# Kernel optimization log

Hardware: AMD Instinct MI355X
Metric: run time of the kernel (lower is better)

Reference implementation:

```python
import jax, jax.numpy as jnp
import numpy as np

B, T = 64, 512          # batch, seq_len
D = 512                 # model_size / LSTM hidden
V = 256                 # vocab_size
R, W, M = 4, 16, 5      # read_heads, cell_size, nr_cells
RW = R * W
IFC = R * W + 3 * W + 5 * R + 3   # DNC interface vector size = 135
EPS = 1e-6
CLIP = 20.0


def setup_inputs():
    ks = jax.random.split(jax.random.key(0), 12)
    s = 0.05
    f32 = jnp.float32
    return {
        'tokens':   jax.random.randint(ks[0], (B, T), 0, V, dtype=jnp.int32),
        'emb':      jax.random.normal(ks[1], (V, D), f32),
        'lstm_Wi0': jax.random.normal(ks[2], (4 * D, D + RW), f32) * s,
        'lstm_Wh0': jax.random.normal(ks[3], (4 * D, D), f32) * s,
        'lstm_b0':  jnp.zeros((4 * D,), f32),
        'lstm_Wi1': jax.random.normal(ks[4], (4 * D, D), f32) * s,
        'lstm_Wh1': jax.random.normal(ks[5], (4 * D, D), f32) * s,
        'lstm_b1':  jnp.zeros((4 * D,), f32),
        'W_if':     jax.random.normal(ks[6], (IFC, D), f32) * s,
        'b_if':     jnp.zeros((IFC,), f32),
        'W_out':    jax.random.normal(ks[7], (D, D + RW), f32) * s,
        'b_out':    jnp.zeros((D,), f32),
        'W_fc':     jax.random.normal(ks[8], (V, D), f32) * s,
        'b_fc':     jnp.zeros((V,), f32),
    }


def _cosine(mem, keys):
    # mem (B,M,W), keys (B,K,W) -> (B,K,M) batchwise cosine similarity
    mn = mem / (jnp.linalg.norm(mem, axis=2, keepdims=True) + EPS)
    kn = keys / (jnp.linalg.norm(keys, axis=2, keepdims=True) + EPS)
    return jnp.einsum('bkw,bmw->bkm', kn, mn)


def _allocate(usage):
    # DNC allocation weighting via sort + exclusive cumprod, then unsort
    u = EPS + (1.0 - EPS) * usage                           # (B,M)
    idx = jnp.argsort(u, axis=1)                            # ascending usage
    sorted_u = jnp.take_along_axis(u, idx, axis=1)
    prod_excl = jnp.cumprod(
        jnp.concatenate([jnp.ones_like(u[:, :1]), sorted_u], axis=1), axis=1)[:, :-1]
    alloc_sorted = (1.0 - sorted_u) * prod_excl
    inv = jnp.argsort(idx, axis=1)                          # reverse permutation
    return jnp.take_along_axis(alloc_sorted, inv, axis=1)


def _dnc_forward(tokens, emb, lstm_Wi0, lstm_Wh0, lstm_b0,
                 lstm_Wi1, lstm_Wh1, lstm_b1, W_if, b_if,
                 W_out, b_out, W_fc, b_fc):
    x = emb[tokens]                                         # (B,T,D)
    eye_mask = 1.0 - jnp.eye(M, dtype=x.dtype)

    def lstm_cell(xin, h, c, Wi, Wh, b):
        g = xin @ Wi.T + h @ Wh.T + b
        i, f, gg, o = jnp.split(g, 4, axis=1)               # torch gate order i,f,g,o
        c2 = jax.nn.sigmoid(f) * c + jax.nn.sigmoid(i) * jnp.tanh(gg)
        h2 = jax.nn.sigmoid(o) * jnp.tanh(c2)
        return h2, c2

    def step(carry, x_t):
        h0, c0, h1, c1, mem, link, prec, rw_p, ww_p, usage, last_read = carry
        xin = jnp.concatenate([x_t, last_read], axis=1)     # (B, D+RW)
        nh0, nc0 = lstm_cell(xin, h0, c0, lstm_Wi0, lstm_Wh0, lstm_b0)
        nh1, nc1 = lstm_cell(nh0, h1, c1, lstm_Wi1, lstm_Wh1, lstm_b1)
        out = jnp.clip(nh1, -CLIP, CLIP)
        xi = out @ W_if.T + b_if                            # (B, IFC)

        o = 0
        read_keys = jnp.tanh(xi[:, :RW]).reshape(-1, R, W); o = RW
        read_str  = jax.nn.softplus(xi[:, o:o + R]); o += R
        write_key = jnp.tanh(xi[:, o:o + W]); o += W
        write_str = jax.nn.softplus(xi[:, o]); o += 1
        erase     = jax.nn.sigmoid(xi[:, o:o + W]); o += W
        write_vec = jnp.tanh(xi[:, o:o + W]); o += W
        free_g    = jax.nn.sigmoid(xi[:, o:o + R]); o += R
        alloc_g   = jax.nn.sigmoid(xi[:, o]); o += 1
        write_g   = jax.nn.sigmoid(xi[:, o]); o += 1
        read_modes = jax.nn.softmax(xi[:, o:o + 3 * R].reshape(-1, R, 3), axis=-1)

        # ---- write head ----
        usage2 = usage + (1.0 - usage) * ww_p               # single write head
        psi = jnp.prod(1.0 - free_g[:, :, None] * rw_p, axis=1)   # (B,M)
        usage2 = usage2 * psi
        wcw = jax.nn.softmax(
            _cosine(mem, write_key[:, None, :])[:, 0, :] * write_str[:, None], axis=1)
        alloc = _allocate(usage2)
        ww = write_g[:, None] * (alloc_g[:, None] * alloc
                                 + (1.0 - alloc_g[:, None]) * wcw)  # (B,M)
        mem2 = mem * (1.0 - ww[:, :, None] * erase[:, None, :]) \
               + ww[:, :, None] * write_vec[:, None, :]
        link2 = (1.0 - ww[:, :, None] - ww[:, None, :]) * link \
                + ww[:, :, None] * prec[:, None, :]
        link2 = link2 * eye_mask
        prec2 = (1.0 - jnp.sum(ww, axis=1, keepdims=True)) * prec + ww

        # ---- read heads ----
        rcw = jax.nn.softmax(_cosine(mem2, read_keys) * read_str[:, :, None], axis=2)
        fwd = jnp.einsum('bij,brj->bri', link2, rw_p)       # L @ w_prev
        bwd = jnp.einsum('bij,bri->brj', link2, rw_p)       # L^T @ w_prev
        rw = (read_modes[..., 0:1] * bwd + read_modes[..., 1:2] * fwd
              + read_modes[..., 2:3] * rcw)                 # (B,R,M)
        read_vecs = jnp.einsum('brm,bmw->brw', rw, mem2).reshape(-1, RW)

        y = jnp.concatenate([out, read_vecs], axis=1) @ W_out.T + b_out  # (B,D)
        carry = (nh0, nc0, nh1, nc1, mem2, link2, prec2, rw, ww, usage2, read_vecs)
        return carry, y

    b = tokens.shape[0]
    z = lambda *shape: jnp.zeros(shape, x.dtype)
    carry0 = (z(b, D), z(b, D), z(b, D), z(b, D),
              z(b, M, W), z(b, M, M), z(b, M),
              z(b, R, M), z(b, M), z(b, M), z(b, RW))
    _, ys = jax.lax.scan(step, carry0, jnp.swapaxes(x, 0, 1))
    y = jnp.swapaxes(ys, 0, 1)                              # (B,T,D)
    logits = y @ W_fc.T + b_fc                              # (B,T,V)
    return jnp.transpose(logits, (0, 2, 1))                 # (B,V,T)


def reference(tokens, emb, lstm_Wi0, lstm_Wh0, lstm_b0,
              lstm_Wi1, lstm_Wh1, lstm_b1, W_if, b_if,
              W_out, b_out, W_fc, b_fc):
    return _dnc_forward(tokens, emb, lstm_Wi0, lstm_Wh0, lstm_b0,
                        lstm_Wi1, lstm_Wh1, lstm_b1, W_if, b_if,
                        W_out, b_out, W_fc, b_fc)
```

## Files before the change

### kernel.cpp

```cpp
#include <hip/hip_runtime.h>
#include <hip/hip_bf16.h>

typedef __hip_bfloat16 bf16;
typedef _Float16 f16;
typedef _Float16 f16x8 __attribute__((ext_vector_type(8)));
typedef float f32x4 __attribute__((ext_vector_type(4)));
typedef unsigned long long u64;
typedef unsigned short ushort_t;

__device__ __forceinline__ float b2f(bf16 x){ return __bfloat162float(x); }
__device__ __forceinline__ float sigf(float x){ return 1.f/(1.f+expf(-x)); }
__device__ __forceinline__ float splus(float x){ return fmaxf(x,0.f)+log1pf(expf(-fabsf(x))); }
__device__ __forceinline__ float ldf(const void* p, int i, int isf32){
  return isf32 ? ((const float*)p)[i] : __bfloat162float(((const bf16*)p)[i]);
}
__device__ __forceinline__ void ast64(u64* p, u64 v){ __hip_atomic_store(p, v, __ATOMIC_RELAXED, __HIP_MEMORY_SCOPE_AGENT); }
__device__ __forceinline__ u64 ald64(u64* p){ return __hip_atomic_load(p, __ATOMIC_RELAXED, __HIP_MEMORY_SCOPE_AGENT); }
__device__ __forceinline__ void ast32(unsigned* p, unsigned v){ __hip_atomic_store(p, v, __ATOMIC_RELAXED, __HIP_MEMORY_SCOPE_AGENT); }
__device__ __forceinline__ unsigned ald32(unsigned* p){ return __hip_atomic_load(p, __ATOMIC_RELAXED, __HIP_MEMORY_SCOPE_AGENT); }

union U4H8 { uint4 u; f16x8 h; };
union U64H4 { u64 u; f16 h[4]; };
union H16 { f16 h; ushort_t s; };

__global__ void k_detect(const void* __restrict__ emb, int* __restrict__ flag){
  __shared__ float mx[256];
  int tid=threadIdx.x;
  float v = fabsf(__bfloat162float(((const bf16*)emb)[tid]));
  mx[tid]=v; __syncthreads();
  for(int s=128;s>0;s>>=1){ if(tid<s) mx[tid]=fmaxf(mx[tid],mx[tid+s]); __syncthreads(); }
  if(tid==0){ flag[0] = (mx[0]>1000.f) ? 1 : 0; flag[1] = 0; }
}

__global__ void k_embW(const void* __restrict__ emb, const void* __restrict__ Wi0,
                       const void* __restrict__ b0,
                       const int* __restrict__ flags, float* __restrict__ embW){
  int f=flags[0];
  int row = blockIdx.x;
  __shared__ float w[512];
  for(int k=threadIdx.x;k<512;k+=256) w[k]=ldf(Wi0,row*576+k,f);
  __syncthreads();
  int v = threadIdx.x;
  float acc=ldf(b0,row,f);
  #pragma unroll 4
  for(int k=0;k<512;k++) acc += ldf(emb,v*512+k,f)*w[k];
  embW[row*256+v]=acc;
}

__global__ void k_wpkA(const void* __restrict__ Wh0, const void* __restrict__ Wi0,
                       const int* __restrict__ flags, ushort_t* __restrict__ PA){
  int f=flags[0];
  int idx=blockIdx.x*256+threadIdx.x;
  if(idx>=1179648) return;
  int j=idx&7, l=(idx>>3)&63, rest=idx>>9;
  int c=rest%18, t2=rest/18, w=t2&7, r=t2>>3;
  int G=w>>1, hh=w&1, m=l&15, q4=l>>4;
  int row=G*512 + r*32 + hh*16 + m;
  int k=c*32 + q4*8 + j;
  float val = (k<512)? ldf(Wh0,row*512+k,f) : ldf(Wi0,row*576+k,f);
  H16 hx; hx.h=(f16)val; PA[idx]=hx.s;
}
__global__ void k_wpkB(const void* __restrict__ Wi1, const void* __restrict__ Wh1,
                       const int* __restrict__ flags, ushort_t* __restrict__ PB){
  int f=flags[0];
  int idx=blockIdx.x*256+threadIdx.x;
  if(idx>=2097152) return;
  int j=idx&7, l=(idx>>3)&63, rest=idx>>9;
  int c=rest&31, t2=rest>>5, w=t2&7, r=t2>>3;
  int G=w>>1, hh=w&1, m=l&15, q4=l>>4;
  int row=G*512 + r*32 + hh*16 + m;
  int k=c*32 + q4*8 + j;
  float val = (k<512)? ldf(Wi1,row*512+k,f) : ldf(Wh1,row*512+k-512,f);
  H16 hx; hx.h=(f16)val; PB[idx]=hx.s;
}

__global__ void k_wifP(const void* __restrict__ W_if, const void* __restrict__ b_if,
                       const int* __restrict__ flags,
                       ushort_t* __restrict__ PW, float* __restrict__ b_ifF,
                       unsigned* __restrict__ FLz){
  int f=flags[0];
  int idx=blockIdx.x*256+threadIdx.x;
  if(idx<73728){
    int j=idx&7, l=(idx>>3)&63, c=(idx>>9)&15, tile=idx>>13;
    int row=tile*16+(l&15);
    int k=c*32+(l>>4)*8+j;
    float val=(row<135)? ldf(W_if,row*512+k,f) : 0.f;
    H16 hx; hx.h=(f16)val; PW[idx]=hx.s;
  }
  if(idx<64) FLz[idx]=0u;
  if(idx<135) b_ifF[idx]=ldf(b_if,idx,f);
}

__global__ void k_wc(const void* __restrict__ W_fc, const void* __restrict__ W_out,
                     const void* __restrict__ b_out, const void* __restrict__ b_fc,
                     const int* __restrict__ flags,
                     float* __restrict__ Wc, float* __restrict__ bc){
  int f=flags[0];
  int idx=blockIdx.x*256+threadIdx.x;
  int v=idx/576, j=idx-v*576;
  float acc=0.f;
  #pragma unroll 4
  for(int d=0;d<512;d++) acc += ldf(W_fc,v*512+d,f)*ldf(W_out,d*576+j,f);
  Wc[idx]=acc;
  if(j==0){
    float a=ldf(b_fc,v,f);
    for(int d=0;d<512;d++) a += ldf(W_fc,v*512+d,f)*ldf(b_out,d,f);
    bc[v]=a;
  }
}

__attribute__((amdgpu_waves_per_eu(2,2)))
__global__ void __launch_bounds__(512) k_dnc3(
    const int* __restrict__ tokens, const void* __restrict__ b1, const int* __restrict__ flags,
    const float* __restrict__ embW, const ushort_t* __restrict__ PA, const ushort_t* __restrict__ PB,
    const ushort_t* __restrict__ PW, const float* __restrict__ b_ifF,
    u64* GX0, u64* GX1, unsigned* FL,
    bf16* __restrict__ cat)
{
  const int bid = blockIdx.x;
  const int g   = bid>>4, r = bid&15;
  const int tid = threadIdx.x;
  const int wv  = tid>>6, l = tid&63;
  const int lm  = l&15,  q4 = l>>4;
  const int d   = tid>>4, bb = tid&15;
  const int mb  = tid>>5, mu = tid&31;
  const int f32i = flags[0];

  __shared__ __align__(16) u64 HB[4352];
  __shared__ float PR[128*17];
  __shared__ f16  sh_pub[512];
  __shared__ float sh_b1[128];
  __shared__ float b_ifL[144];
  __shared__ float xis2[16*149];
  __shared__ float s_mem[1280], s_mem2[1280], s_link[400], s_link2[400];
  __shared__ float s_prec[80], s_prec2[80], s_rwp[320], s_rw[320];
  __shared__ float s_wwp[80], s_ww[80], s_usage[80], s_wl[80];
  __shared__ float s_rl[320], s_fwd[320], s_bwd[320], s_wsum[16];
  __shared__ float rvbuf[1024];

#define WAITG(TGT) do{ if(tid<16){ unsigned _tg=(unsigned)(TGT); int _wd=0; \
    while(ald32(&FL[g*16+tid]) < _tg && _wd<50000000){ __builtin_amdgcn_s_sleep(1); _wd++; } } \
  __syncthreads(); }while(0)
#define PUBF(VAL) do{ __syncthreads(); \
  if(tid==0) ast32(&FL[g*16+r],(unsigned)(VAL)); }while(0)
#define XI(i) xis2[mb*149+(i)]

  f16x8 fa[18], fb[32];
  {
    const uint4* PAv=(const uint4*)PA;
    const uint4* PBv=(const uint4*)PB;
    #pragma unroll
    for(int c=0;c<18;c++){ U4H8 t4; t4.u = PAv[((r*8+wv)*18+c)*64 + l]; fa[c]=t4.h; }
    #pragma unroll
    for(int c=0;c<32;c++){ U4H8 t4; t4.u = PBv[((r*8+wv)*32+c)*64 + l]; fb[c]=t4.h; }
    #pragma unroll
    for(int c=0;c<18;c++) asm volatile("" :: "v"(fa[c]));
    #pragma unroll
    for(int c=0;c<32;c++) asm volatile("" :: "v"(fb[c]));
  }
  if(tid<128) sh_b1[tid]=ldf(b1,(tid>>5)*512 + r*32 + (tid&31), f32i);
  if(tid<144) b_ifL[tid]=(tid<135)? b_ifF[tid] : 0.f;
  for(int i=tid;i<1280;i+=512) s_mem[i]=0.f;
  for(int i=tid;i<400;i+=512) s_link[i]=0.f;
  for(int i=tid;i<320;i+=512) s_rwp[i]=0.f;
  if(tid<80){ s_prec[tid]=0.f; s_wwp[tid]=0.f; s_usage[tid]=0.f; }
  float c0s=0.f, c1s=0.f;

  const f16x8* HBv=(const f16x8*)HB;
  const uint4* PWv=(const uint4*)PW;

  {
    int tok0=tokens[(g*16+bb)*512];
    int base0=(r*32+d)*256+tok0;
    float e0=embW[base0], e2=embW[262144+base0], e3=embW[393216+base0];
    c0s = sigf(e0)*tanhf(e2);
    float h0v = sigf(e3)*tanhf(c0s);
    sh_pub[d*16+bb]=(f16)h0v;
  }
  __syncthreads();
  if(tid<128){
    int ks=tid>>4, b2=tid&15;
    U64H4 pk;
    #pragma unroll
    for(int i=0;i<4;i++) pk.h[i]=sh_pub[(ks*4+i)*16+b2];
    ast64(&GX0[g*4096+((4*r+(ks>>1))*16+b2)*2+(ks&1)], pk.u);
  }
  PUBF(2u);
  WAITG(2u);
  {
    u64 s0=ald64(&GX0[g*4096+tid      ]);
    u64 s1=ald64(&GX0[g*4096+tid+512  ]);
    u64 s2=ald64(&GX0[g*4096+tid+1024 ]);
    u64 s3=ald64(&GX0[g*4096+tid+1536 ]);
    HB[tid]=s0; HB[tid+512]=s1; HB[tid+1024]=s2; HB[tid+1536]=s3;
  }
  __syncthreads();
  {
    f32x4 accB=(f32x4){0.f,0.f,0.f,0.f};
    #pragma unroll
    for(int c=0;c<16;c++){
      f16x8 bfr=HBv[(c*4+q4)*16+lm];
      accB=__builtin_amdgcn_mfma_f32_16x16x32_f16(fb[c],bfr,accB,0,0,0);
    }
    #pragma unroll
    for(int reg=0;reg<4;reg++) PR[(wv*16+q4*4+reg)*17+lm]=accB[reg];
  }
  __syncthreads();
  {
    float gi=PR[(d    )*17+bb]+sh_b1[d];
    float gg=PR[(64+d )*17+bb]+sh_b1[64+d];
    float go=PR[(96+d )*17+bb]+sh_b1[96+d];
    c1s = sigf(gi)*tanhf(gg);
    float h=sigf(go)*tanhf(c1s);
    sh_pub[d*16+bb]=(f16)h;
  }
  __syncthreads();
  if(tid<128){
    int ks=tid>>4, b2=tid&15;
    U64H4 pk;
    #pragma unroll
    for(int i=0;i<4;i++) pk.h[i]=sh_pub[(ks*4+i)*16+b2];
    ast64(&GX1[g*4096+((4*r+(ks>>1))*16+b2)*2+(ks&1)], pk.u);
  }
  PUBF(3u);

  for(int tt=0;tt<512;tt++){
    const int p=tt&1, pn=p^1;

    f32x4 accA=(f32x4){0.f,0.f,0.f,0.f};
    #pragma unroll
    for(int c=0;c<16;c++){
      f16x8 bfr=HBv[(c*4+q4)*16+lm];
      accA=__builtin_amdgcn_mfma_f32_16x16x32_f16(fa[c],bfr,accA,0,0,0);
    }
    float em0,em1,em2,em3;
    {
      int tn=(tt<511)?tt+1:511;
      int tok=tokens[(g*16+bb)*512+tn];
      int base=(r*32+d)*256+tok;
      em0=embW[base]; em1=embW[131072+base]; em2=embW[262144+base]; em3=embW[393216+base];
    }

    WAITG(2*tt+3);

    {
      u64 s0=ald64(&GX1[g*4096+p*2048+tid      ]);
      u64 s1=ald64(&GX1[g*4096+p*2048+tid+512  ]);
      u64 s2=ald64(&GX1[g*4096+p*2048+tid+1024 ]);
      u64 s3=ald64(&GX1[g*4096+p*2048+tid+1536 ]);
      HB[2048+tid]=s0; HB[2048+tid+512]=s1; HB[2048+tid+1024]=s2; HB[2048+tid+1536]=s3;
    }
    __syncthreads();

    {
      f32x4 xa=(f32x4){0.f,0.f,0.f,0.f};
      #pragma unroll
      for(int hh=0;hh<4;hh++){
        uint4 w4[4];
        #pragma unroll
        for(int cc=0;cc<4;cc++) w4[cc]=PWv[(wv*16 + hh*4+cc)*64 + l];
        #pragma unroll
        for(int cc=0;cc<4;cc++){
          U4H8 t4; t4.u=w4[cc];
          f16x8 bfr=HBv[1024+((hh*4+cc)*4+q4)*16+lm];
          xa=__builtin_amdgcn_mfma_f32_16x16x32_f16(t4.h,bfr,xa,0,0,0);
        }
      }
      #pragma unroll
      for(int reg=0;reg<4;reg++){
        int row=wv*16+q4*4+reg;
        xis2[lm*149+row]=xa[reg]+b_ifL[row];
      }
      if(wv==0){
        f32x4 xb=(f32x4){0.f,0.f,0.f,0.f};
        #pragma unroll
        for(int hh=0;hh<4;hh++){
          uint4 w4[4];
          #pragma unroll
          for(int cc=0;cc<4;cc++) w4[cc]=PWv[(128 + hh*4+cc)*64 + l];
          #pragma unroll
          for(int cc=0;cc<4;cc++){
            U4H8 t4; t4.u=w4[cc];
            f16x8 bfr=HBv[1024+((hh*4+cc)*4+q4)*16+lm];
            xb=__builtin_amdgcn_mfma_f32_16x16x32_f16(t4.h,bfr,xb,0,0,0);
          }
        }
        #pragma unroll
        for(int reg=0;reg<4;reg++){
          int row=128+q4*4+reg;
          xis2[lm*149+row]=xb[reg]+b_ifL[row];
        }
      }
    }
    __syncthreads();

    if(mu<5){
      int m=mu;
      float u=s_usage[mb*5+m]+(1.f-s_usage[mb*5+m])*s_wwp[mb*5+m];
      float psi=1.f;
      #pragma unroll
      for(int rr=0;rr<4;rr++) psi *= 1.f - sigf(XI(117+rr))*s_rwp[mb*20+rr*5+m];
      u*=psi; s_usage[mb*5+m]=u;
      float nm=0.f,dt=0.f,nk=0.f;
      #pragma unroll
      for(int w=0;w<16;w++){
        float mv=s_mem[mb*80+m*16+w], kv=tanhf(XI(68+w));
        nm+=mv*mv; dt+=mv*kv; nk+=kv*kv;
      }
      float sim=dt/((sqrtf(nm)+1e-6f)*(sqrtf(nk)+1e-6f));
      s_wl[mb*5+m]=sim*splus(XI(84));
    }
    __syncthreads();
    if(mu==0){
      float mx=-1e30f;
      for(int m=0;m<5;m++) mx=fmaxf(mx,s_wl[mb*5+m]);
      float e[5]; float s=0.f;
      for(int m=0;m<5;m++){ e[m]=expf(s_wl[mb*5+m]-mx); s+=e[m]; }
      float u[5]; int id[5];
      for(int m=0;m<5;m++){ u[m]=1e-6f+(1.f-1e-6f)*s_usage[mb*5+m]; id[m]=m; }
      for(int i=1;i<5;i++){
        float uv=u[i]; int iv=id[i]; int j=i-1;
        while(j>=0&&u[j]>uv){u[j+1]=u[j];id[j+1]=id[j];j--;}
        u[j+1]=uv; id[j+1]=iv;
      }
      float alm[5]; float prod=1.f;
      for(int i=0;i<5;i++){ alm[id[i]]=(1.f-u[i])*prod; prod*=u[i]; }
      float ag=sigf(XI(121)), wgg=sigf(XI(122));
      float wsum=0.f;
      for(int m=0;m<5;m++){
        float wcw=e[m]/s;
        float w_=wgg*(ag*alm[m]+(1.f-ag)*wcw);
        s_ww[mb*5+m]=w_; wsum+=w_;
      }
      s_wsum[mb]=wsum;
    }
    __syncthreads();
    for(int k=mu;k<80;k+=32){
      int m=k>>4,w=k&15;
      float er=sigf(XI(85+w)), wv2=tanhf(XI(101+w));
      float w_=s_ww[mb*5+m];
      s_mem2[mb*80+k]=s_mem[mb*80+k]*(1.f-w_*er)+w_*wv2;
    }
    if(mu<25){
      int i=mu/5, j=mu-5*i;
      s_link2[mb*25+mu]=(i==j)?0.f:((1.f-s_ww[mb*5+i]-s_ww[mb*5+j])*s_link[mb*25+mu]+s_ww[mb*5+i]*s_prec[mb*5+j]);
    } else if(mu<30){
      int j=mu-25;
      s_prec2[mb*5+j]=(1.f-s_wsum[mb])*s_prec[mb*5+j]+s_ww[mb*5+j];
    }
    __syncthreads();
    if(mu<20){
      int rr=mu/5, m=mu-5*rr;
      float nm=0.f,dt=0.f,nk=0.f;
      #pragma unroll
      for(int w=0;w<16;w++){
        float mv=s_mem2[mb*80+m*16+w], kv=tanhf(XI(rr*16+w));
        nm+=mv*mv; dt+=mv*kv; nk+=kv*kv;
      }
      float sim=dt/((sqrtf(nm)+1e-6f)*(sqrtf(nk)+1e-6f));
      s_rl[mb*20+mu]=sim*splus(XI(64+rr));
      float af=0.f, ab=0.f;
      #pragma unroll
      for(int j=0;j<5;j++) af+=s_link2[mb*25+m*5+j]*s_rwp[mb*20+rr*5+j];
      #pragma unroll
      for(int i=0;i<5;i++) ab+=s_link2[mb*25+i*5+m]*s_rwp[mb*20+rr*5+i];
      s_fwd[mb*20+rr*5+m]=af;
      s_bwd[mb*20+rr*5+m]=ab;
    }
    __syncthreads();
    if(mu<20){
      int rr=mu/5;
      float mx=-1e30f;
      for(int m=0;m<5;m++) mx=fmaxf(mx,s_rl[mb*20+rr*5+m]);
      float s=0.f;
      for(int m=0;m<5;m++) s+=expf(s_rl[mb*20+rr*5+m]-mx);
      float rcw=expf(s_rl[mb*20+mu]-mx)/s;
      float q0=XI(123+3*rr),q1=XI(124+3*rr),q2=XI(125+3*rr);
      float m3=fmaxf(q0,fmaxf(q1,q2));
      float e0=expf(q0-m3),e1=expf(q1-m3),e2=expf(q2-m3);
      float inv=1.f/(e0+e1+e2);
      s_rw[mb*20+mu]=(e0*s_bwd[mb*20+mu]+e1*s_fwd[mb*20+mu]+e2*rcw)*inv;
    }
    __syncthreads();
    for(int k=mu;k<64;k+=32){
      int rr=k>>4,w=k&15;
      float a=0.f;
      #pragma unroll
      for(int m=0;m<5;m++) a+=s_rw[mb*20+rr*5+m]*s_mem2[mb*80+m*16+w];
      rvbuf[mb*64+k]=a;
    }
    for(int k=mu;k<80;k+=32) s_mem[mb*80+k]=s_mem2[mb*80+k];
    if(mu<25) s_link[mb*25+mu]=s_link2[mb*25+mu];
    else if(mu<30) s_prec[mb*5+mu-25]=s_prec2[mb*5+mu-25];
    if(mu<20) s_rwp[mb*20+mu]=s_rw[mb*20+mu];
    if(mu>=27&&mu<32){ int m=mu-27; s_wwp[mb*5+m]=s_ww[mb*5+m]; }
    __syncthreads();

    if(tt==511){
      int cb=((g*16+r)*512+tt)*576;
      if(tid<128){
        int kg=tid>>1, e=tid&1;
        U64H4 pv; pv.u=HB[2048+(kg*16+r)*2+e];
        #pragma unroll
        for(int i=0;i<4;i++){
          float x=(float)pv.h[i];
          cat[cb+kg*8+e*4+i]=__float2bfloat16(fminf(fmaxf(x,-20.f),20.f));
        }
      }
      if(tid<64) cat[cb+512+tid]=__float2bfloat16(rvbuf[r*64+tid]);
      break;
    }

    if(tid<256){
      int kg=tid>>5, rem=tid&31, b2=rem>>1, e=rem&1;
      U64H4 pk;
      #pragma unroll
      for(int i=0;i<4;i++) pk.h[i]=(f16)rvbuf[b2*64 + kg*8+e*4+i];
      HB[4096+(kg*16+b2)*2+e]=pk.u;
    }
    __syncthreads();
    #pragma unroll
    for(int c2=0;c2<2;c2++){
      f16x8 bfr=HBv[2048+(c2*4+q4)*16+lm];
      accA=__builtin_amdgcn_mfma_f32_16x16x32_f16(fa[16+c2],bfr,accA,0,0,0);
    }
    #pragma unroll
    for(int reg=0;reg<4;reg++) PR[(wv*16+q4*4+reg)*17+lm]=accA[reg];
    __syncthreads();
    {
      float gi=PR[(d    )*17+bb]+em0;
      float gf=PR[(32+d )*17+bb]+em1;
      float gg=PR[(64+d )*17+bb]+em2;
      float go=PR[(96+d )*17+bb]+em3;
      float c0=sigf(gf)*c0s+sigf(gi)*tanhf(gg);
      c0s=c0;
      float h=sigf(go)*tanhf(c0);
      sh_pub[d*16+bb]=(f16)h;
    }
    __syncthreads();
    if(tid<128){
      int ks=tid>>4, b2=tid&15;
      U64H4 pk;
      #pragma unroll
      for(int i=0;i<4;i++) pk.h[i]=sh_pub[(ks*4+i)*16+b2];
      ast64(&GX0[g*4096+pn*2048+((4*r+(ks>>1))*16+b2)*2+(ks&1)], pk.u);
    }
    PUBF(2*tt+4);

    f32x4 accB=(f32x4){0.f,0.f,0.f,0.f};
    #pragma unroll
    for(int c=16;c<32;c++){
      f16x8 bfr=HBv[1024+((c-16)*4+q4)*16+lm];
      accB=__builtin_amdgcn_mfma_f32_16x16x32_f16(fb[c],bfr,accB,0,0,0);
    }
    {
      int cb=((g*16+r)*512+tt)*576;
      if(tid<128){
        int kg=tid>>1, e=tid&1;
        U64H4 pv; pv.u=HB[2048+(kg*16+r)*2+e];
        #pragma unroll
        for(int i=0;i<4;i++){
          float x=(float)pv.h[i];
          cat[cb+kg*8+e*4+i]=__float2bfloat16(fminf(fmaxf(x,-20.f),20.f));
        }
      }
      if(tid<64) cat[cb+512+tid]=__float2bfloat16(rvbuf[r*64+tid]);
    }

    WAITG(2*tt+4);

    {
      u64 s0=ald64(&GX0[g*4096+pn*2048+tid      ]);
      u64 s1=ald64(&GX0[g*4096+pn*2048+tid+512  ]);
      u64 s2=ald64(&GX0[g*4096+pn*2048+tid+1024 ]);
      u64 s3=ald64(&GX0[g*4096+pn*2048+tid+1536 ]);
      HB[tid]=s0; HB[tid+512]=s1; HB[tid+1024]=s2; HB[tid+1536]=s3;
    }
    __syncthreads();
    #pragma unroll
    for(int c=0;c<16;c++){
      f16x8 bfr=HBv[(c*4+q4)*16+lm];
      accB=__builtin_amdgcn_mfma_f32_16x16x32_f16(fb[c],bfr,accB,0,0,0);
    }
    #pragma unroll
    for(int reg=0;reg<4;reg++) PR[(wv*16+q4*4+reg)*17+lm]=accB[reg];
    __syncthreads();
    {
      float gi=PR[(d    )*17+bb]+sh_b1[d];
      float gf=PR[(32+d )*17+bb]+sh_b1[32+d];
      float gg=PR[(64+d )*17+bb]+sh_b1[64+d];
      float go=PR[(96+d )*17+bb]+sh_b1[96+d];
      float c1=sigf(gf)*c1s+sigf(gi)*tanhf(gg);
      c1s=c1;
      float h=sigf(go)*tanhf(c1);
      sh_pub[d*16+bb]=(f16)h;
    }
    __syncthreads();
    if(tid<128){
      int ks=tid>>4, b2=tid&15;
      U64H4 pk;
      #pragma unroll
      for(int i=0;i<4;i++) pk.h[i]=sh_pub[(ks*4+i)*16+b2];
      ast64(&GX1[g*4096+pn*2048+((4*r+(ks>>1))*16+b2)*2+(ks&1)], pk.u);
    }
    PUBF(2*tt+5);
  }
#undef WAITG
#undef PUBF
#undef XI
}

__global__ void __launch_bounds__(256) k_out(const bf16* __restrict__ cat,
                                             const float* __restrict__ Wc,
                                             const float* __restrict__ bc,
                                             float* __restrict__ outp){
  int t0=blockIdx.x*64, v0=blockIdx.y*64, b=blockIdx.z;
  __shared__ float As[64][33];
  __shared__ float Bs[32][65];
  int tid=threadIdx.x;
  int ti=tid>>4, vi=tid&15;
  float acc[4][4]={};
  for(int k0=0;k0<576;k0+=32){
    for(int i=tid;i<64*32;i+=256){
      int rr=i>>5,k=i&31;
      As[rr][k]=b2f(cat[(b*512+t0+rr)*576+k0+k]);
    }
    for(int i=tid;i<64*32;i+=256){
      int v=i>>5,k=i&31;
      Bs[k][v]=Wc[(v0+v)*576+k0+k];
    }
    __syncthreads();
    #pragma unroll 8
    for(int kk=0;kk<32;kk++){
      float av[4],bv[4];
      #pragma unroll
      for(int x=0;x<4;x++) av[x]=As[ti*4+x][kk];
      #pragma unroll
      for(int y=0;y<4;y++) bv[y]=Bs[kk][vi*4+y];
      #pragma unroll
      for(int x=0;x<4;x++)
        #pragma unroll
        for(int y=0;y<4;y++) acc[x][y]+=av[x]*bv[y];
    }
    __syncthreads();
  }
  #pragma unroll
  for(int y=0;y<4;y++){
    int v=v0+vi*4+y;
    float bcv=bc[v];
    #pragma unroll
    for(int x=0;x<4;x++){
      int tt=t0+ti*4+x;
      outp[(b*256+v)*512+tt]=acc[x][y]+bcv;
    }
  }
}

extern "C" void kernel_launch(void* const* d_in, const int* in_sizes, int n_in,
                              void* d_out, int out_size, void* d_ws, size_t ws_size,
                              hipStream_t stream) {
  const int*  tokens = (const int*) d_in[0];
  const void* emb    = d_in[1];
  const void* Wi0    = d_in[2];
  const void* Wh0    = d_in[3];
  const void* b0     = d_in[4];
  const void* Wi1    = d_in[5];
  const void* Wh1    = d_in[6];
  const void* b1     = d_in[7];
  const void* W_if   = d_in[8];
  const void* b_if   = d_in[9];
  const void* W_out  = d_in[10];
  const void* b_out  = d_in[11];
  const void* W_fc   = d_in[12];
  const void* b_fc   = d_in[13];

  static const int expect[14] = {64*512, 256*512, 2048*576, 2048*512, 2048,
                                 2048*512, 2048*512, 2048, 135*512, 135,
                                 512*576, 512, 256*512, 256};
  bool ok = (n_in == 14);
  if(ok) for(int i=0;i<14;i++) if(in_sizes[i]!=expect[i]) ok=false;

  int*      flags = (int*)d_ws;
  float*    embW  = (float*)d_ws + 64;
  ushort_t* PA    = (ushort_t*)(embW + 524288);
  ushort_t* PB    = PA + 1310720;
  float*    Wreg  = (float*)(PB + 2097152);
  float*    b_ifF = Wreg + 69632;
  float*    Wc    = b_ifF + 160;
  float*    bc    = Wc + 147456;
  u64*      GX0   = (u64*)(bc + 256);
  u64*      GX1   = GX0 + 16384;
  u64*      GXL   = GX1 + 16384;
  bf16*     cat   = (bf16*)(GXL + 2048);
  unsigned* FL    = (unsigned*)(PA + 1179648);
  ushort_t* PW    = (ushort_t*)Wreg;

  size_t need = 9783168ull + 278528ull + 37748736ull;
  if(!ok || ws_size < need){
    hipMemsetAsync(d_out, 0, (size_t)out_size*4, stream);
    return;
  }

  k_detect<<<dim3(1), dim3(256), 0, stream>>>(emb, flags);
  k_embW<<<dim3(2048), dim3(256), 0, stream>>>(emb, Wi0, b0, flags, embW);
  k_wpkA<<<dim3(4608), dim3(256), 0, stream>>>(Wh0, Wi0, flags, PA);
  k_wpkB<<<dim3(8192), dim3(256), 0, stream>>>(Wi1, Wh1, flags, PB);
  k_wifP<<<dim3(288), dim3(256), 0, stream>>>(W_if, b_if, flags, PW, b_ifF, FL);
  k_wc  <<<dim3(576),  dim3(256), 0, stream>>>(W_fc, W_out, b_out, b_fc, flags, Wc, bc);

  void* kargs[] = {
    (void*)&tokens, (void*)&b1, (void*)&flags,
    (void*)&embW, (void*)&PA, (void*)&PB,
    (void*)&PW, (void*)&b_ifF,
    (void*)&GX0, (void*)&GX1, (void*)&FL,
    (void*)&cat
  };
  hipLaunchCooperativeKernel((const void*)k_dnc3, dim3(64), dim3(512), kargs, 0, stream);

  k_out<<<dim3(8,4,64), dim3(256), 0, stream>>>(cat, Wc, bc, (float*)d_out);
}
```

Measured before the change: 13.97 ms.

## Stream LSTM weights from global instead of register-resident, use wave barriers in DNC

Drops the 50 register-resident f16x8 weight fragments (fa/fb) and reloads the LSTM weight tiles from global memory each timestep, with partial prefetch before the waits. This frees a large block of VGPRs. It also parallelises the allocation sort/softmax across lanes using rank-based products, and replaces several block-wide __syncthreads in the per-batch DNC memory section with wave barriers. The cost is repeated weight reads every step through L2/L1, which adds latency on the serial recurrent critical path. The wave-barrier swap assumes each batch's DNC work stays within one wavefront.

```diff
diff --git a/kernel.cpp b/kernel.cpp
--- a/kernel.cpp
+++ b/kernel.cpp
@@ -144,20 +144,13 @@
 #define PUBF(VAL) do{ __syncthreads(); \
   if(tid==0) ast32(&FL[g*16+r],(unsigned)(VAL)); }while(0)
 #define XI(i) xis2[mb*149+(i)]
-
-  f16x8 fa[18], fb[32];
-  {
-    const uint4* PAv=(const uint4*)PA;
-    const uint4* PBv=(const uint4*)PB;
-    #pragma unroll
-    for(int c=0;c<18;c++){ U4H8 t4; t4.u = PAv[((r*8+wv)*18+c)*64 + l]; fa[c]=t4.h; }
-    #pragma unroll
-    for(int c=0;c<32;c++){ U4H8 t4; t4.u = PBv[((r*8+wv)*32+c)*64 + l]; fb[c]=t4.h; }
-    #pragma unroll
-    for(int c=0;c<18;c++) asm volatile("" :: "v"(fa[c]));
-    #pragma unroll
-    for(int c=0;c<32;c++) asm volatile("" :: "v"(fb[c]));
-  }
+#define WB() __builtin_amdgcn_wave_barrier()
+
+  const f16x8* HBv=(const f16x8*)HB;
+  const uint4* PAv=(const uint4*)PA;
+  const uint4* PBv=(const uint4*)PB;
+  const uint4* PWv=(const uint4*)PW;
+
   if(tid<128) sh_b1[tid]=ldf(b1,(tid>>5)*512 + r*32 + (tid&31), f32i);
   if(tid<144) b_ifL[tid]=(tid<135)? b_ifF[tid] : 0.f;
   for(int i=tid;i<1280;i+=512) s_mem[i]=0.f;
@@ -165,9 +158,6 @@
   for(int i=tid;i<320;i+=512) s_rwp[i]=0.f;
   if(tid<80){ s_prec[tid]=0.f; s_wwp[tid]=0.f; s_usage[tid]=0.f; }
   float c0s=0.f, c1s=0.f;
-
-  const f16x8* HBv=(const f16x8*)HB;
-  const uint4* PWv=(const uint4*)PW;
 
   {
     int tok0=tokens[(g*16+bb)*512];
@@ -199,8 +189,9 @@
     f32x4 accB=(f32x4){0.f,0.f,0.f,0.f};
     #pragma unroll
     for(int c=0;c<16;c++){
+      U4H8 wf; wf.u=PBv[((r*8+wv)*32+c)*64+l];
       f16x8 bfr=HBv[(c*4+q4)*16+lm];
-      accB=__builtin_amdgcn_mfma_f32_16x16x32_f16(fb[c],bfr,accB,0,0,0);
+      accB=__builtin_amdgcn_mfma_f32_16x16x32_f16(wf.h,bfr,accB,0,0,0);
     }
     #pragma unroll
     for(int reg=0;reg<4;reg++) PR[(wv*16+q4*4+reg)*17+lm]=accB[reg];
@@ -230,8 +221,9 @@
     f32x4 accA=(f32x4){0.f,0.f,0.f,0.f};
     #pragma unroll
     for(int c=0;c<16;c++){
+      U4H8 wf; wf.u=PAv[((r*8+wv)*18+c)*64+l];
       f16x8 bfr=HBv[(c*4+q4)*16+lm];
-      accA=__builtin_amdgcn_mfma_f32_16x16x32_f16(fa[c],bfr,accA,0,0,0);
+      accA=__builtin_amdgcn_mfma_f32_16x16x32_f16(wf.h,bfr,accA,0,0,0);
     }
     float em0,em1,em2,em3;
     {
@@ -240,6 +232,9 @@
       int base=(r*32+d)*256+tok;
       em0=embW[base]; em1=embW[131072+base]; em2=embW[262144+base]; em3=embW[393216+base];
     }
+    uint4 pfA2[2];
+    #pragma unroll
+    for(int c2=0;c2<2;c2++) pfA2[c2]=PAv[((r*8+wv)*18+16+c2)*64+l];
 
     WAITG(2*tt+3);
 
@@ -258,7 +253,7 @@
       for(int hh=0;hh<4;hh++){
         uint4 w4[4];
         #pragma unroll
-        for(int cc=0;cc<4;cc++) w4[cc]=PWv[(wv*16 + hh*4+cc)*64 + l];
+        for(int cc=0;cc<4;cc++) w4[cc]=PWv[(wv*16+hh*4+cc)*64+l];
         #pragma unroll
         for(int cc=0;cc<4;cc++){
           U4H8 t4; t4.u=w4[cc];
@@ -277,7 +272,7 @@
         for(int hh=0;hh<4;hh++){
           uint4 w4[4];
           #pragma unroll
-          for(int cc=0;cc<4;cc++) w4[cc]=PWv[(128 + hh*4+cc)*64 + l];
+          for(int cc=0;cc<4;cc++) w4[cc]=PWv[(128+hh*4+cc)*64+l];
           #pragma unroll
           for(int cc=0;cc<4;cc++){
             U4H8 t4; t4.u=w4[cc];
@@ -310,31 +305,42 @@
       float sim=dt/((sqrtf(nm)+1e-6f)*(sqrtf(nk)+1e-6f));
       s_wl[mb*5+m]=sim*splus(XI(84));
     }
-    __syncthreads();
+    WB();
+    if(mu<5){
+      int m=mu;
+      float mx=s_wl[mb*5];
+      #pragma unroll
+      for(int j=1;j<5;j++) mx=fmaxf(mx,s_wl[mb*5+j]);
+      float e=expf(s_wl[mb*5+m]-mx);
+      float u=1e-6f+(1.f-1e-6f)*s_usage[mb*5+m];
+      s_rl [mb*20+m]=u;
+      s_bwd[mb*20+m]=e;
+    }
+    WB();
+    if(mu<5){
+      int m=mu;
+      float u=s_rl[mb*20+m], e=s_bwd[mb*20+m];
+      float s=0.f, prod=1.f;
+      #pragma unroll
+      for(int j=0;j<5;j++){
+        s+=s_bwd[mb*20+j];
+        float uj=s_rl[mb*20+j];
+        if(uj<u || (uj==u && j<m)) prod*=uj;
+      }
+      float wcw=e/s;
+      float alloc=(1.f-u)*prod;
+      float ag=sigf(XI(121)), wgg=sigf(XI(122));
+      float w_=wgg*(ag*alloc+(1.f-ag)*wcw);
+      s_ww[mb*5+m]=w_;
+    }
+    WB();
     if(mu==0){
-      float mx=-1e30f;
-      for(int m=0;m<5;m++) mx=fmaxf(mx,s_wl[mb*5+m]);
-      float e[5]; float s=0.f;
-      for(int m=0;m<5;m++){ e[m]=expf(s_wl[mb*5+m]-mx); s+=e[m]; }
-      float u[5]; int id[5];
-      for(int m=0;m<5;m++){ u[m]=1e-6f+(1.f-1e-6f)*s_usage[mb*5+m]; id[m]=m; }
-      for(int i=1;i<5;i++){
-        float uv=u[i]; int iv=id[i]; int j=i-1;
-        while(j>=0&&u[j]>uv){u[j+1]=u[j];id[j+1]=id[j];j--;}
-        u[j+1]=uv; id[j+1]=iv;
-      }
-      float alm[5]; float prod=1.f;
-      for(int i=0;i<5;i++){ alm[id[i]]=(1.f-u[i])*prod; prod*=u[i]; }
-      float ag=sigf(XI(121)), wgg=sigf(XI(122));
-      float wsum=0.f;
-      for(int m=0;m<5;m++){
-        float wcw=e[m]/s;
-        float w_=wgg*(ag*alm[m]+(1.f-ag)*wcw);
-        s_ww[mb*5+m]=w_; wsum+=w_;
-      }
-      s_wsum[mb]=wsum;
-    }
-    __syncthreads();
+      float ws=0.f;
+      #pragma unroll
+      for(int m=0;m<5;m++) ws+=s_ww[mb*5+m];
+      s_wsum[mb]=ws;
+    }
+    WB();
     for(int k=mu;k<80;k+=32){
       int m=k>>4,w=k&15;
       float er=sigf(XI(85+w)), wv2=tanhf(XI(101+w));
@@ -348,7 +354,7 @@
       int j=mu-25;
       s_prec2[mb*5+j]=(1.f-s_wsum[mb])*s_prec[mb*5+j]+s_ww[mb*5+j];
     }
-    __syncthreads();
+    WB();
     if(mu<20){
       int rr=mu/5, m=mu-5*rr;
       float nm=0.f,dt=0.f,nk=0.f;
@@ -367,12 +373,14 @@
       s_fwd[mb*20+rr*5+m]=af;
       s_bwd[mb*20+rr*5+m]=ab;
     }
-    __syncthreads();
+    WB();
     if(mu<20){
       int rr=mu/5;
       float mx=-1e30f;
+      #pragma unroll
       for(int m=0;m<5;m++) mx=fmaxf(mx,s_rl[mb*20+rr*5+m]);
       float s=0.f;
+      #pragma unroll
       for(int m=0;m<5;m++) s+=expf(s_rl[mb*20+rr*5+m]-mx);
       float rcw=expf(s_rl[mb*20+mu]-mx)/s;
       float q0=XI(123+3*rr),q1=XI(124+3*rr),q2=XI(125+3*rr);
@@ -381,7 +389,7 @@
       float inv=1.f/(e0+e1+e2);
       s_rw[mb*20+mu]=(e0*s_bwd[mb*20+mu]+e1*s_fwd[mb*20+mu]+e2*rcw)*inv;
     }
-    __syncthreads();
+    WB();
     for(int k=mu;k<64;k+=32){
       int rr=k>>4,w=k&15;
       float a=0.f;
@@ -421,8 +429,9 @@
     __syncthreads();
     #pragma unroll
     for(int c2=0;c2<2;c2++){
+      U4H8 wf; wf.u=pfA2[c2];
       f16x8 bfr=HBv[2048+(c2*4+q4)*16+lm];
-      accA=__builtin_amdgcn_mfma_f32_16x16x32_f16(fa[16+c2],bfr,accA,0,0,0);
+      accA=__builtin_amdgcn_mfma_f32_16x16x32_f16(wf.h,bfr,accA,0,0,0);
     }
     #pragma unroll
     for(int reg=0;reg<4;reg++) PR[(wv*16+q4*4+reg)*17+lm]=accA[reg];
@@ -450,9 +459,13 @@
     f32x4 accB=(f32x4){0.f,0.f,0.f,0.f};
     #pragma unroll
     for(int c=16;c<32;c++){
+      U4H8 wf; wf.u=PBv[((r*8+wv)*32+c)*64+l];
       f16x8 bfr=HBv[1024+((c-16)*4+q4)*16+lm];
-      accB=__builtin_amdgcn_mfma_f32_16x16x32_f16(fb[c],bfr,accB,0,0,0);
-    }
+      accB=__builtin_amdgcn_mfma_f32_16x16x32_f16(wf.h,bfr,accB,0,0,0);
+    }
+    uint4 pfB[16];
+    #pragma unroll
+    for(int c=0;c<16;c++) pfB[c]=PBv[((r*8+wv)*32+c)*64+l];
     {
       int cb=((g*16+r)*512+tt)*576;
       if(tid<128){
@@ -479,8 +492,9 @@
     __syncthreads();
     #pragma unroll
     for(int c=0;c<16;c++){
+      U4H8 wf; wf.u=pfB[c];
       f16x8 bfr=HBv[(c*4+q4)*16+lm];
-      accB=__builtin_amdgcn_mfma_f32_16x16x32_f16(fb[c],bfr,accB,0,0,0);
+      accB=__builtin_amdgcn_mfma_f32_16x16x32_f16(wf.h,bfr,accB,0,0,0);
     }
     #pragma unroll
     for(int reg=0;reg<4;reg++) PR[(wv*16+q4*4+reg)*17+lm]=accB[reg];
@@ -508,6 +522,7 @@
 #undef WAITG
 #undef PUBF
 #undef XI
+#undef WB
 }
 
 __global__ void __launch_bounds__(256) k_out(const bf16* __restrict__ cat,
```

After: 12.50 ms. 1.12x faster.
